# Optimization experiments

Measured on AMD Instinct MI355X. Metric: run time of the kernel, lower is better.

The kernel has to match this reference:

```python
import jax, jax.numpy as jnp
import numpy as np


def setup_inputs() -> dict:
    key = jax.random.key(0)
    ks = jax.random.split(key, 7)
    B, S, D = 256, 1024, 128  # batch of sets, set size, n_input
    H = 256
    x = jax.random.normal(ks[0], (B, S, D), dtype=jnp.float32)
    # torch nn.Linear weights: [out_features, in_features], in = 2*layer_in
    W0 = jax.random.normal(ks[1], (H, 2 * D), dtype=jnp.float32) * 0.05
    b0 = jnp.zeros((H,), dtype=jnp.float32)
    W1 = jax.random.normal(ks[2], (H, 2 * H), dtype=jnp.float32) * 0.05
    b1 = jnp.zeros((H,), dtype=jnp.float32)
    W2 = jax.random.normal(ks[3], (H, 2 * H), dtype=jnp.float32) * 0.05
    b2 = jnp.zeros((H,), dtype=jnp.float32)
    return {"x": x, "W0": W0, "b0": b0, "W1": W1, "b1": b1, "W2": W2, "b2": b2}


def reference(x, W0, b0, W1, b1, W2, b2):
    # x: [B, S, D] batch of sets. Original loops over batch; we vmap.
    def apply_set(y):
        # y: [S, d]
        for W, b in ((W0, b0), (W1, b1), (W2, b2)):
            mean = jnp.mean(y, axis=0, keepdims=True)            # [1, d]
            mean = jnp.broadcast_to(mean, y.shape)               # [S, d]
            z = jnp.concatenate([y, mean], axis=1)               # [S, 2d]
            y = jnp.tanh(z @ W.T + b)                            # [S, out]
        return jnp.mean(y, axis=0)                               # [out]
    return jax.vmap(apply_set)(x)                                # [B, out]
```

## Files before the change

kernel.cpp:

```cpp
#include <hip/hip_runtime.h>
#include <hip/hip_bf16.h>

#define B_ 256
#define S_ 1024
#define D_ 128
#define H_ 256

typedef short short8 __attribute__((ext_vector_type(8)));
typedef float f32x4 __attribute__((ext_vector_type(4)));

__device__ unsigned short g_Wb0[H_ * D_];
__device__ unsigned short g_Wb1[H_ * H_];
__device__ unsigned short g_Wb2[H_ * H_];
__device__ float g_mean0[B_ * D_];
__device__ float g_colsum1[B_ * H_];
__device__ float g_colsum2[B_ * H_];

__device__ __forceinline__ unsigned short f2bf(float x) {
    union { float f; unsigned u; } v; v.f = x;
    unsigned r = v.u + 0x7FFFu + ((v.u >> 16) & 1u);
    return (unsigned short)(r >> 16);
}
__device__ __forceinline__ float bf2f(unsigned short h) {
    union { float f; unsigned u; } v; v.u = ((unsigned)h) << 16;
    return v.f;
}
__device__ __forceinline__ float fast_tanh(float x) {
    float e = __builtin_amdgcn_exp2f(x * 2.885390081777927f);
    float r = __builtin_amdgcn_rcpf(1.0f + e);
    return 1.0f - 2.0f * r;
}

__global__ __launch_bounds__(256) void prep_kernel(
    const float* __restrict__ W0, const float* __restrict__ W1,
    const float* __restrict__ W2)
{
    int i = blockIdx.x * 256 + threadIdx.x;
    if (i < H_ * D_) { g_Wb0[i] = f2bf(W0[(i >> 7) * 256 + (i & 127)]); return; }
    i -= H_ * D_;
    if (i < H_ * H_) { g_Wb1[i] = f2bf(W1[(i >> 8) * 512 + (i & 255)]); return; }
    i -= H_ * H_;
    if (i < H_ * H_) { g_Wb2[i] = f2bf(W2[(i >> 8) * 512 + (i & 255)]); return; }
}

__global__ __launch_bounds__(1024) void means0_kernel(const float* __restrict__ x)
{
    const int set = blockIdx.x, t = threadIdx.x;
    const int cg = t & 31, rg = t >> 5;
    const float* xb = x + (size_t)set * S_ * D_;
    f32x4 s = (f32x4){0.f, 0.f, 0.f, 0.f};
    #pragma unroll 8
    for (int i = 0; i < 32; ++i)
        s += *(const f32x4*)(xb + (rg + i * 32) * D_ + cg * 4);
    __shared__ f32x4 red[32][32];
    red[rg][cg] = s;
    __syncthreads();
    if (t < 32) {
        f32x4 a = red[0][t];
        #pragma unroll
        for (int g = 1; g < 32; ++g) a += red[g][t];
        #pragma unroll
        for (int c = 0; c < 4; ++c) g_mean0[set * D_ + t * 4 + c] = a[c];
    }
}

template <int LAYER>
__global__ __launch_bounds__(512, 2) void layer_kernel(
    const float* __restrict__ x, const float* __restrict__ W,
    const float* __restrict__ bias, unsigned short* __restrict__ y,
    float* __restrict__ out)
{
    constexpr int K  = (LAYER == 0) ? D_ : H_;
    constexpr int KS = K / 32;
    constexpr int SLOTS = K / 8;
    const int set = blockIdx.x;
    const int t = threadIdx.x;
    const int lane = t & 63, wave = t >> 6;
    const int l15 = lane & 15, quad = lane >> 4;

    __shared__ unsigned short W_lds[256 * K];
    __shared__ float mean_lds[K];
    __shared__ float c_lds[H_];
    __shared__ float colsum_lds[H_];
    __shared__ float cpart[512];

    const unsigned short* Wb = (LAYER == 0) ? g_Wb0 : (LAYER == 1) ? g_Wb1 : g_Wb2;
    const float* msrc = (LAYER == 0) ? g_mean0 : (LAYER == 1) ? g_colsum1 : g_colsum2;

    if (t < K)   mean_lds[t] = msrc[set * K + t] * (1.f / S_);
    if (t < H_)  colsum_lds[t] = 0.f;
    __syncthreads();

    {
        const int n = t >> 1, h = t & 1;
        #pragma unroll
        for (int i = 0; i < SLOTS / 2; ++i) {
            const int slot = h * (SLOTS / 2) + i;
            *(uint4*)(&W_lds[n * K + ((slot ^ (n & 7)) * 8)]) =
                *(const uint4*)(&Wb[n * K + slot * 8]);
        }
    }
    {
        const int j = t >> 1, h = t & 1;
        const float* wl = W + j * 2 * K + h * (K / 2);
        const float* wr = wl + K;
        float acc = 0.f;
        #pragma unroll 4
        for (int k = 0; k < K / 2; k += 4) {
            f32x4 a = *(const f32x4*)(wl + k);
            f32x4 b = *(const f32x4*)(wr + k);
            f32x4 m = *(const f32x4*)(&mean_lds[h * (K / 2) + k]);
            #pragma unroll
            for (int c = 0; c < 4; ++c)
                acc += m[c] * (b[c] + (a[c] - bf2f(f2bf(a[c]))));
        }
        cpart[t] = acc;
    }
    __syncthreads();
    if (t < H_) c_lds[t] = bias[t] + cpart[2 * t] + cpart[2 * t + 1];
    __syncthreads();

    for (int half = 0; half < 2; ++half) {
        const int rowbase = half * 512 + wave * 64;

        short8 a[4][KS];
        if (LAYER == 0) {
            const float* xb = x + ((size_t)set * S_ + rowbase) * D_;
            #pragma unroll
            for (int mf = 0; mf < 4; ++mf)
                #pragma unroll
                for (int ks = 0; ks < KS; ++ks) {
                    const float* p = xb + (mf * 16 + l15) * D_ + ks * 32 + quad * 8;
                    f32x4 v0 = *(const f32x4*)(p);
                    f32x4 v1 = *(const f32x4*)(p + 4);
                    short8 sv;
                    #pragma unroll
                    for (int c = 0; c < 4; ++c) {
                        sv[c]     = (short)f2bf(v0[c]);
                        sv[4 + c] = (short)f2bf(v1[c]);
                    }
                    a[mf][ks] = sv;
                }
        } else {
            const unsigned short* yb = y + ((size_t)set * S_ + rowbase) * H_;
            #pragma unroll
            for (int mf = 0; mf < 4; ++mf)
                #pragma unroll
                for (int ks = 0; ks < KS; ++ks)
                    a[mf][ks] = *(const short8*)(yb + (mf * 16 + l15) * H_ + ks * 32 + quad * 8);
        }

        for (int nt = 0; nt < 8; ++nt) {
            f32x4 acc[4][2];
            #pragma unroll
            for (int i = 0; i < 4; ++i) {
                acc[i][0] = (f32x4){0.f, 0.f, 0.f, 0.f};
                acc[i][1] = (f32x4){0.f, 0.f, 0.f, 0.f};
            }
            const int r0 = (nt * 32 + l15) * K;
            const int r1 = (nt * 32 + 16 + l15) * K;
            #pragma unroll
            for (int ks = 0; ks < KS; ++ks) {
                const int so = (((ks * 4 + quad) ^ (l15 & 7)) * 8);
                short8 b0 = *(const short8*)(&W_lds[r0 + so]);
                short8 b1 = *(const short8*)(&W_lds[r1 + so]);
                #pragma unroll
                for (int mf = 0; mf < 4; ++mf)
                    acc[mf][0] = __builtin_amdgcn_mfma_f32_16x16x32_bf16(a[mf][ks], b0, acc[mf][0], 0, 0, 0);
                #pragma unroll
                for (int mf = 0; mf < 4; ++mf)
                    acc[mf][1] = __builtin_amdgcn_mfma_f32_16x16x32_bf16(a[mf][ks], b1, acc[mf][1], 0, 0, 0);
            }
            #pragma unroll
            for (int nf = 0; nf < 2; ++nf) {
                const int col = nt * 32 + nf * 16 + l15;
                const float cv = c_lds[col];
                float sn = 0.f;
                #pragma unroll
                for (int mf = 0; mf < 4; ++mf) {
                    #pragma unroll
                    for (int r = 0; r < 4; ++r) {
                        float th = fast_tanh(acc[mf][nf][r] + cv);
                        sn += th;
                        if (LAYER < 2)
                            y[((size_t)set * S_ + rowbase + mf * 16 + quad * 4 + r) * H_ + col] = f2bf(th);
                    }
                }
                sn += __shfl_xor(sn, 16);
                sn += __shfl_xor(sn, 32);
                if (quad == 0) atomicAdd(&colsum_lds[col], sn);
            }
        }
    }
    __syncthreads();
    if (t < H_) {
        if (LAYER == 2) out[set * H_ + t] = colsum_lds[t] * (1.f / S_);
        else if (LAYER == 1) g_colsum2[set * H_ + t] = colsum_lds[t];
        else g_colsum1[set * H_ + t] = colsum_lds[t];
    }
}

extern "C" void kernel_launch(void* const* d_in, const int* in_sizes, int n_in,
                              void* d_out, int out_size, void* d_ws, size_t ws_size,
                              hipStream_t stream) {
    (void)in_sizes; (void)n_in; (void)out_size; (void)ws_size;
    const float* x  = (const float*)d_in[0];
    const float* W0 = (const float*)d_in[1];
    const float* b0 = (const float*)d_in[2];
    const float* W1 = (const float*)d_in[3];
    const float* b1 = (const float*)d_in[4];
    const float* W2 = (const float*)d_in[5];
    const float* b2 = (const float*)d_in[6];
    float* out = (float*)d_out;
    unsigned short* ws = (unsigned short*)d_ws;

    prep_kernel<<<dim3(640), dim3(256), 0, stream>>>(W0, W1, W2);
    means0_kernel<<<dim3(256), dim3(1024), 0, stream>>>(x);
    layer_kernel<0><<<dim3(256), dim3(512), 0, stream>>>(x, W0, b0, ws, out);
    layer_kernel<1><<<dim3(256), dim3(512), 0, stream>>>(x, W1, b1, ws, out);
    layer_kernel<2><<<dim3(256), dim3(512), 0, stream>>>(x, W2, b2, ws, out);
}
```

Measured before the change: 443.0 us.

## Split each set across two 1024-thread blocks with atomic colsum reduction

Each layer kernel now runs 512 blocks of 1024 threads, with each block covering half of a set's rows, and partial column sums are combined through global atomics. The prep kernel zeroes those accumulators and the output. The MFMA operand order is swapped so each lane holds four contiguous output columns, which allows packed bf16 stores via v_cvt_pk_bf16_f32 and a vectorized epilogue. The A-fragments are loaded before the bias-correction pass so load latency can overlap it. In exchange, every block reloads the full weight matrix into LDS, which doubles weight traffic, and the global float atomics make the output reduction order nondeterministic.

```diff
diff --git a/kernel.cpp b/kernel.cpp
--- a/kernel.cpp
+++ b/kernel.cpp
@@ -1,5 +1,4 @@
 #include <hip/hip_runtime.h>
-#include <hip/hip_bf16.h>
 
 #define B_ 256
 #define S_ 1024
@@ -30,10 +29,15 @@
     float r = __builtin_amdgcn_rcpf(1.0f + e);
     return 1.0f - 2.0f * r;
 }
+__device__ __forceinline__ unsigned cvt_pk_bf16(float lo, float hi) {
+    unsigned r;
+    asm("v_cvt_pk_bf16_f32 %0, %1, %2" : "=v"(r) : "v"(lo), "v"(hi));
+    return r;
+}
 
 __global__ __launch_bounds__(256) void prep_kernel(
     const float* __restrict__ W0, const float* __restrict__ W1,
-    const float* __restrict__ W2)
+    const float* __restrict__ W2, float* __restrict__ out)
 {
     int i = blockIdx.x * 256 + threadIdx.x;
     if (i < H_ * D_) { g_Wb0[i] = f2bf(W0[(i >> 7) * 256 + (i & 127)]); return; }
@@ -41,6 +45,12 @@
     if (i < H_ * H_) { g_Wb1[i] = f2bf(W1[(i >> 8) * 512 + (i & 255)]); return; }
     i -= H_ * H_;
     if (i < H_ * H_) { g_Wb2[i] = f2bf(W2[(i >> 8) * 512 + (i & 255)]); return; }
+    i -= H_ * H_;
+    if (i < B_ * H_) { g_colsum1[i] = 0.f; return; }
+    i -= B_ * H_;
+    if (i < B_ * H_) { g_colsum2[i] = 0.f; return; }
+    i -= B_ * H_;
+    if (i < B_ * H_) { out[i] = 0.f; return; }
 }
 
 __global__ __launch_bounds__(1024) void means0_kernel(const float* __restrict__ x)
@@ -65,7 +75,7 @@
 }
 
 template <int LAYER>
-__global__ __launch_bounds__(512, 2) void layer_kernel(
+__global__ __launch_bounds__(1024, 4) void layer_kernel(
     const float* __restrict__ x, const float* __restrict__ W,
     const float* __restrict__ bias, unsigned short* __restrict__ y,
     float* __restrict__ out)
@@ -73,7 +83,8 @@
     constexpr int K  = (LAYER == 0) ? D_ : H_;
     constexpr int KS = K / 32;
     constexpr int SLOTS = K / 8;
-    const int set = blockIdx.x;
+    const int set = blockIdx.x >> 1;
+    const int rh  = blockIdx.x & 1;
     const int t = threadIdx.x;
     const int lane = t & 63, wave = t >> 6;
     const int l15 = lane & 15, quad = lane >> 4;
@@ -82,7 +93,7 @@
     __shared__ float mean_lds[K];
     __shared__ float c_lds[H_];
     __shared__ float colsum_lds[H_];
-    __shared__ float cpart[512];
+    __shared__ float cpart[1024];
 
     const unsigned short* Wb = (LAYER == 0) ? g_Wb0 : (LAYER == 1) ? g_Wb1 : g_Wb2;
     const float* msrc = (LAYER == 0) ? g_mean0 : (LAYER == 1) ? g_colsum1 : g_colsum2;
@@ -92,111 +103,121 @@
     __syncthreads();
 
     {
-        const int n = t >> 1, h = t & 1;
-        #pragma unroll
-        for (int i = 0; i < SLOTS / 2; ++i) {
-            const int slot = h * (SLOTS / 2) + i;
+        const int n = t >> 2, p = t & 3;
+        #pragma unroll
+        for (int i = 0; i < SLOTS / 4; ++i) {
+            const int slot = p * (SLOTS / 4) + i;
             *(uint4*)(&W_lds[n * K + ((slot ^ (n & 7)) * 8)]) =
                 *(const uint4*)(&Wb[n * K + slot * 8]);
         }
     }
+
+    const int rowbase = rh * 512 + wave * 32;
+    short8 a[2][KS];
+    if (LAYER == 0) {
+        const float* xb = x + ((size_t)set * S_ + rowbase) * D_;
+        #pragma unroll
+        for (int mf = 0; mf < 2; ++mf)
+            #pragma unroll
+            for (int ks = 0; ks < KS; ++ks) {
+                const float* p = xb + (mf * 16 + l15) * D_ + ks * 32 + quad * 8;
+                f32x4 v0 = *(const f32x4*)(p);
+                f32x4 v1 = *(const f32x4*)(p + 4);
+                union { short8 s; unsigned u[4]; } sv;
+                sv.u[0] = cvt_pk_bf16(v0[0], v0[1]);
+                sv.u[1] = cvt_pk_bf16(v0[2], v0[3]);
+                sv.u[2] = cvt_pk_bf16(v1[0], v1[1]);
+                sv.u[3] = cvt_pk_bf16(v1[2], v1[3]);
+                a[mf][ks] = sv.s;
+            }
+    } else {
+        const unsigned short* yb = y + ((size_t)set * S_ + rowbase) * H_;
+        #pragma unroll
+        for (int mf = 0; mf < 2; ++mf)
+            #pragma unroll
+            for (int ks = 0; ks < KS; ++ks)
+                a[mf][ks] = *(const short8*)(yb + (mf * 16 + l15) * H_ + ks * 32 + quad * 8);
+    }
+
     {
-        const int j = t >> 1, h = t & 1;
-        const float* wl = W + j * 2 * K + h * (K / 2);
+        const int j = t >> 2, q = t & 3;
+        const float* wl = W + j * 2 * K + q * (K / 4);
         const float* wr = wl + K;
         float acc = 0.f;
         #pragma unroll 4
-        for (int k = 0; k < K / 2; k += 4) {
-            f32x4 a = *(const f32x4*)(wl + k);
-            f32x4 b = *(const f32x4*)(wr + k);
-            f32x4 m = *(const f32x4*)(&mean_lds[h * (K / 2) + k]);
+        for (int k = 0; k < K / 4; k += 4) {
+            f32x4 aa = *(const f32x4*)(wl + k);
+            f32x4 bb = *(const f32x4*)(wr + k);
+            f32x4 m  = *(const f32x4*)(&mean_lds[q * (K / 4) + k]);
             #pragma unroll
             for (int c = 0; c < 4; ++c)
-                acc += m[c] * (b[c] + (a[c] - bf2f(f2bf(a[c]))));
+                acc += m[c] * (bb[c] + (aa[c] - bf2f(f2bf(aa[c]))));
         }
         cpart[t] = acc;
     }
     __syncthreads();
-    if (t < H_) c_lds[t] = bias[t] + cpart[2 * t] + cpart[2 * t + 1];
-    __syncthreads();
-
-    for (int half = 0; half < 2; ++half) {
-        const int rowbase = half * 512 + wave * 64;
-
-        short8 a[4][KS];
-        if (LAYER == 0) {
-            const float* xb = x + ((size_t)set * S_ + rowbase) * D_;
-            #pragma unroll
-            for (int mf = 0; mf < 4; ++mf)
+    if (t < H_) c_lds[t] = bias[t] + cpart[4 * t] + cpart[4 * t + 1]
+                                   + cpart[4 * t + 2] + cpart[4 * t + 3];
+    __syncthreads();
+
+    unsigned short* ybase = y + ((size_t)set * S_ + rowbase) * H_;
+
+    for (int nt = 0; nt < 8; ++nt) {
+        f32x4 acc[2][2];
+        #pragma unroll
+        for (int i = 0; i < 2; ++i) {
+            acc[i][0] = (f32x4){0.f, 0.f, 0.f, 0.f};
+            acc[i][1] = (f32x4){0.f, 0.f, 0.f, 0.f};
+        }
+        const int r0 = (nt * 32 + l15) * K;
+        const int r1 = r0 + 16 * K;
+        #pragma unroll
+        for (int ks = 0; ks < KS; ++ks) {
+            const int so = (((ks * 4 + quad) ^ (l15 & 7)) * 8);
+            short8 w0 = *(const short8*)(&W_lds[r0 + so]);
+            short8 w1 = *(const short8*)(&W_lds[r1 + so]);
+            acc[0][0] = __builtin_amdgcn_mfma_f32_16x16x32_bf16(w0, a[0][ks], acc[0][0], 0, 0, 0);
+            acc[1][0] = __builtin_amdgcn_mfma_f32_16x16x32_bf16(w0, a[1][ks], acc[1][0], 0, 0, 0);
+            acc[0][1] = __builtin_amdgcn_mfma_f32_16x16x32_bf16(w1, a[0][ks], acc[0][1], 0, 0, 0);
+            acc[1][1] = __builtin_amdgcn_mfma_f32_16x16x32_bf16(w1, a[1][ks], acc[1][1], 0, 0, 0);
+        }
+        #pragma unroll
+        for (int nf = 0; nf < 2; ++nf) {
+            const int colbase = nt * 32 + nf * 16 + quad * 4;
+            const f32x4 cv = *(const f32x4*)(&c_lds[colbase]);
+            f32x4 cs = (f32x4){0.f, 0.f, 0.f, 0.f};
+            #pragma unroll
+            for (int mf = 0; mf < 2; ++mf) {
+                f32x4 th;
                 #pragma unroll
-                for (int ks = 0; ks < KS; ++ks) {
-                    const float* p = xb + (mf * 16 + l15) * D_ + ks * 32 + quad * 8;
-                    f32x4 v0 = *(const f32x4*)(p);
-                    f32x4 v1 = *(const f32x4*)(p + 4);
-                    short8 sv;
-                    #pragma unroll
-                    for (int c = 0; c < 4; ++c) {
-                        sv[c]     = (short)f2bf(v0[c]);
-                        sv[4 + c] = (short)f2bf(v1[c]);
-                    }
-                    a[mf][ks] = sv;
+                for (int r = 0; r < 4; ++r)
+                    th[r] = fast_tanh(acc[mf][nf][r] + cv[r]);
+                cs += th;
+                if (LAYER < 2) {
+                    uint2 pv;
+                    pv.x = cvt_pk_bf16(th[0], th[1]);
+                    pv.y = cvt_pk_bf16(th[2], th[3]);
+                    *(uint2*)(&ybase[(mf * 16 + l15) * H_ + colbase]) = pv;
                 }
-        } else {
-            const unsigned short* yb = y + ((size_t)set * S_ + rowbase) * H_;
-            #pragma unroll
-            for (int mf = 0; mf < 4; ++mf)
+            }
+            #pragma unroll
+            for (int s = 1; s < 16; s <<= 1) {
                 #pragma unroll
-                for (int ks = 0; ks < KS; ++ks)
-                    a[mf][ks] = *(const short8*)(yb + (mf * 16 + l15) * H_ + ks * 32 + quad * 8);
-        }
-
-        for (int nt = 0; nt < 8; ++nt) {
-            f32x4 acc[4][2];
-            #pragma unroll
-            for (int i = 0; i < 4; ++i) {
-                acc[i][0] = (f32x4){0.f, 0.f, 0.f, 0.f};
-                acc[i][1] = (f32x4){0.f, 0.f, 0.f, 0.f};
-            }
-            const int r0 = (nt * 32 + l15) * K;
-            const int r1 = (nt * 32 + 16 + l15) * K;
-            #pragma unroll
-            for (int ks = 0; ks < KS; ++ks) {
-                const int so = (((ks * 4 + quad) ^ (l15 & 7)) * 8);
-                short8 b0 = *(const short8*)(&W_lds[r0 + so]);
-                short8 b1 = *(const short8*)(&W_lds[r1 + so]);
+                for (int r = 0; r < 4; ++r) cs[r] += __shfl_xor(cs[r], s);
+            }
+            if (l15 == 0) {
                 #pragma unroll
-                for (int mf = 0; mf < 4; ++mf)
-                    acc[mf][0] = __builtin_amdgcn_mfma_f32_16x16x32_bf16(a[mf][ks], b0, acc[mf][0], 0, 0, 0);
-                #pragma unroll
-                for (int mf = 0; mf < 4; ++mf)
-                    acc[mf][1] = __builtin_amdgcn_mfma_f32_16x16x32_bf16(a[mf][ks], b1, acc[mf][1], 0, 0, 0);
-            }
-            #pragma unroll
-            for (int nf = 0; nf < 2; ++nf) {
-                const int col = nt * 32 + nf * 16 + l15;
-                const float cv = c_lds[col];
-                float sn = 0.f;
-                #pragma unroll
-                for (int mf = 0; mf < 4; ++mf) {
-                    #pragma unroll
-                    for (int r = 0; r < 4; ++r) {
-                        float th = fast_tanh(acc[mf][nf][r] + cv);
-                        sn += th;
-                        if (LAYER < 2)
-                            y[((size_t)set * S_ + rowbase + mf * 16 + quad * 4 + r) * H_ + col] = f2bf(th);
-                    }
-                }
-                sn += __shfl_xor(sn, 16);
-                sn += __shfl_xor(sn, 32);
-                if (quad == 0) atomicAdd(&colsum_lds[col], sn);
+                for (int r = 0; r < 4; ++r)
+                    atomicAdd(&colsum_lds[colbase + r], cs[r]);
             }
         }
     }
     __syncthreads();
     if (t < H_) {
-        if (LAYER == 2) out[set * H_ + t] = colsum_lds[t] * (1.f / S_);
-        else if (LAYER == 1) g_colsum2[set * H_ + t] = colsum_lds[t];
-        else g_colsum1[set * H_ + t] = colsum_lds[t];
+        const float v = colsum_lds[t];
+        if (LAYER == 2)      atomicAdd(&out[set * H_ + t], v * (1.f / S_));
+        else if (LAYER == 1) atomicAdd(&g_colsum2[set * H_ + t], v);
+        else                 atomicAdd(&g_colsum1[set * H_ + t], v);
     }
 }
 
@@ -214,9 +235,9 @@
     float* out = (float*)d_out;
     unsigned short* ws = (unsigned short*)d_ws;
 
-    prep_kernel<<<dim3(640), dim3(256), 0, stream>>>(W0, W1, W2);
+    prep_kernel<<<dim3(1408), dim3(256), 0, stream>>>(W0, W1, W2, out);
     means0_kernel<<<dim3(256), dim3(1024), 0, stream>>>(x);
-    layer_kernel<0><<<dim3(256), dim3(512), 0, stream>>>(x, W0, b0, ws, out);
-    layer_kernel<1><<<dim3(256), dim3(512), 0, stream>>>(x, W1, b1, ws, out);
-    layer_kernel<2><<<dim3(256), dim3(512), 0, stream>>>(x, W2, b2, ws, out);
-}
+    layer_kernel<0><<<dim3(512), dim3(1024), 0, stream>>>(x, W0, b0, ws, out);
+    layer_kernel<1><<<dim3(512), dim3(1024), 0, stream>>>(x, W1, b1, ws, out);
+    layer_kernel<2><<<dim3(512), dim3(1024), 0, stream>>>(x, W2, b2, ws, out);
+}
```

Result: slower. 500.2 us (+12.9%).
